# Kernel optimization log

Hardware: AMD Instinct MI355X
Metric: run time of the kernel (lower is better)

Reference implementation:

```python
import jax, jax.numpy as jnp
import numpy as np

N_NODES = 500_000
N_GRAPHS = 8192
HIDDEN = 256


def setup_inputs() -> dict:
    key = jax.random.key(0)
    k1, k2, k3, k4, k5, k6, k7 = jax.random.split(key, 7)
    h = jax.random.normal(k1, (N_NODES, HIDDEN), dtype=jnp.float32)
    node_mult = jax.random.uniform(k2, (N_NODES,), dtype=jnp.float32) * 3.0 + 0.5
    pressure = jax.random.uniform(k3, (N_GRAPHS,), dtype=jnp.float32) * 300.0
    attn_weight = jax.random.normal(k4, (HIDDEN,), dtype=jnp.float32) * (1.0 / np.sqrt(HIDDEN))
    attn_bias = jax.random.normal(k5, (1,), dtype=jnp.float32) * 0.01
    W_pressure = jax.random.normal(k6, (HIDDEN,), dtype=jnp.float32) * 0.02
    batch = jnp.sort(jax.random.randint(k7, (N_NODES,), 0, N_GRAPHS, dtype=jnp.int32))
    return {
        "h": h,
        "node_mult": node_mult,
        "pressure": pressure,
        "attn_weight": attn_weight,
        "attn_bias": attn_bias,
        "W_pressure": W_pressure,
        "batch": batch,
        "n_graphs": N_GRAPHS,
    }


def reference(h, node_mult, pressure, attn_weight, attn_bias, W_pressure, batch, n_graphs):
    # h: [N, H], node_mult: [N], batch: [N] int segment ids, pressure: [G]
    # Multiplicity-weighted mean pool
    total_mult = jax.ops.segment_sum(node_mult, batch, num_segments=n_graphs)  # [G]
    total_mult = jnp.maximum(total_mult, 1e-8)
    w_mean = node_mult / total_mult[batch]  # [N]
    mean_pool = jax.ops.segment_sum(h * w_mean[:, None], batch, num_segments=n_graphs)  # [G, H]

    # Segment max pool (empty segments -> -inf, matching torch full(-inf) init)
    max_pool = jax.ops.segment_max(h, batch, num_segments=n_graphs)  # [G, H]

    # Attention scores with log-multiplicity bias, then segment softmax
    raw_scores = h @ attn_weight + attn_bias[0] + jnp.log(jnp.maximum(node_mult, 1.0))  # [N]
    seg_max = jax.ops.segment_max(raw_scores, batch, num_segments=n_graphs)  # [G]
    exp_s = jnp.exp(raw_scores - seg_max[batch])  # [N]
    denom = jax.ops.segment_sum(exp_s, batch, num_segments=n_graphs)  # [G]
    attn_w = exp_s / denom[batch]  # [N]
    attn_pool = jax.ops.segment_sum(h * attn_w[:, None], batch, num_segments=n_graphs)  # [G, H]

    combined_mean = 0.5 * (mean_pool + attn_pool)  # [G, H]
    p_norm = (pressure / 300.0)[:, None]  # [G, 1]
    combined_mean = combined_mean + p_norm * W_pressure[None, :]
    return jnp.concatenate([combined_mean, max_pool], axis=-1)  # [G, 2H]
```

## Files before the change

### kernel.cpp

```cpp
#include <hip/hip_runtime.h>
#include <math.h>

#define HIDDEN 256
#define CHUNK 8

typedef float fx4 __attribute__((ext_vector_type(4)));

__global__ __launch_bounds__(256) void seg_starts_kernel(
    const int* __restrict__ batch, int* __restrict__ starts, int N, int G) {
  int i = blockIdx.x * blockDim.x + threadIdx.x;
  if (i >= N) return;
  int b = batch[i];
  int prev = (i == 0) ? -1 : batch[i - 1];
  for (int g = prev + 1; g <= b; ++g) starts[g] = i;
  if (i == N - 1) {
    for (int g = b + 1; g <= G; ++g) starts[g] = N;
  }
}

__global__ __launch_bounds__(256) void pool_kernel(
    const float* __restrict__ h, const float* __restrict__ node_mult,
    const float* __restrict__ pressure, const float* __restrict__ attn_weight,
    const float* __restrict__ attn_bias, const float* __restrict__ W_pressure,
    const int* __restrict__ starts, float* __restrict__ out, int G) {
  const int wave = threadIdx.x >> 6;
  const int lane = threadIdx.x & 63;
  const int g = blockIdx.x * 4 + wave;
  if (g >= G) return;

  const int start = starts[g];
  const int end = starts[g + 1];

  const fx4 w4 = *reinterpret_cast<const fx4*>(attn_weight + 4 * lane);
  const float bias = attn_bias[0];

  fx4 attn  = (fx4)(0.f);
  fx4 meanv = (fx4)(0.f);
  fx4 maxv  = (fx4)(-INFINITY);
  float m = -INFINITY;
  float denom = 0.f;
  float tmult = 0.f;

  int i = start;
  for (; i + CHUNK <= end; i += CHUNK) {
    fx4 hv[CHUNK];
    float mult[CHUNK];
#pragma unroll
    for (int j = 0; j < CHUNK; ++j) {
      hv[j] = __builtin_nontemporal_load(
          reinterpret_cast<const fx4*>(h + (size_t)(i + j) * HIDDEN + 4 * lane));
      mult[j] = node_mult[i + j];
    }

    float p[CHUNK];
#pragma unroll
    for (int j = 0; j < CHUNK; ++j)
      p[j] = hv[j].x * w4.x + hv[j].y * w4.y + hv[j].z * w4.z + hv[j].w * w4.w;

#pragma unroll
    for (int off = 32; off >= 1; off >>= 1) {
#pragma unroll
      for (int j = 0; j < CHUNK; ++j) p[j] += __shfl_xor(p[j], off, 64);
    }

    float s[CHUNK];
#pragma unroll
    for (int j = 0; j < CHUNK; ++j)
      s[j] = p[j] + bias + __logf(fmaxf(mult[j], 1.f));

    float cmax = s[0];
#pragma unroll
    for (int j = 1; j < CHUNK; ++j) cmax = fmaxf(cmax, s[j]);

    if (cmax > m) {
      const float scale = __expf(m - cmax);
      denom *= scale;
      attn *= scale;
      m = cmax;
    }

#pragma unroll
    for (int j = 0; j < CHUNK; ++j) {
      const float e = __expf(s[j] - m);
      denom += e;
      attn += hv[j] * e;
      meanv += hv[j] * mult[j];
      maxv.x = fmaxf(maxv.x, hv[j].x);  maxv.y = fmaxf(maxv.y, hv[j].y);
      maxv.z = fmaxf(maxv.z, hv[j].z);  maxv.w = fmaxf(maxv.w, hv[j].w);
      tmult += mult[j];
    }
  }

  for (; i < end; ++i) {
    const fx4 hv = __builtin_nontemporal_load(
        reinterpret_cast<const fx4*>(h + (size_t)i * HIDDEN + 4 * lane));
    const float mult = node_mult[i];

    float p = hv.x * w4.x + hv.y * w4.y + hv.z * w4.z + hv.w * w4.w;
#pragma unroll
    for (int off = 32; off >= 1; off >>= 1) p += __shfl_xor(p, off, 64);

    const float score = p + bias + __logf(fmaxf(mult, 1.f));

    if (score > m) {
      const float scale = __expf(m - score);
      denom *= scale;
      attn *= scale;
      m = score;
    }
    const float e = __expf(score - m);
    denom += e;
    attn += hv * e;
    meanv += hv * mult;
    maxv.x = fmaxf(maxv.x, hv.x);  maxv.y = fmaxf(maxv.y, hv.y);
    maxv.z = fmaxf(maxv.z, hv.z);  maxv.w = fmaxf(maxv.w, hv.w);
    tmult += mult;
  }

  const float inv_tm  = 1.f / fmaxf(tmult, 1e-8f);
  const float inv_den = (denom > 0.f) ? 1.f / denom : 0.f;
  const float p_norm  = pressure[g] * (1.f / 300.f);
  const fx4 wp4 = *reinterpret_cast<const fx4*>(W_pressure + 4 * lane);

  fx4 res = 0.5f * (meanv * inv_tm + attn * inv_den) + p_norm * wp4;

  float* outg = out + (size_t)g * (2 * HIDDEN);
  *reinterpret_cast<fx4*>(outg + 4 * lane) = res;
  *reinterpret_cast<fx4*>(outg + HIDDEN + 4 * lane) = maxv;
}

extern "C" void kernel_launch(void* const* d_in, const int* in_sizes, int n_in,
                              void* d_out, int out_size, void* d_ws, size_t ws_size,
                              hipStream_t stream) {
  const float* h           = (const float*)d_in[0];
  const float* node_mult   = (const float*)d_in[1];
  const float* pressure    = (const float*)d_in[2];
  const float* attn_weight = (const float*)d_in[3];
  const float* attn_bias   = (const float*)d_in[4];
  const float* W_pressure  = (const float*)d_in[5];
  const int*   batch       = (const int*)d_in[6];

  const int N = in_sizes[1];
  const int G = in_sizes[2];

  int* starts = (int*)d_ws;
  float* out = (float*)d_out;

  seg_starts_kernel<<<(N + 255) / 256, 256, 0, stream>>>(batch, starts, N, G);
  pool_kernel<<<(G + 3) / 4, 256, 0, stream>>>(h, node_mult, pressure,
                                               attn_weight, attn_bias,
                                               W_pressure, starts, out, G);
}
```

Before: 103.7 us.

## Split each segment across two waves and merge partial softmax states in LDS

Each graph segment is now handled by two waves, each covering half of the full 8-node chunks. The partial online-softmax, mean, max and multiplicity state is merged through shared memory after a block barrier. The scalar tail loop is replaced by one padded, masked chunk processed by the first wave. This doubles the waves in flight to hide memory latency on an HBM-bound reduction, at the cost of a barrier, LDS traffic and uneven work between the two halves.

Result: faster. 100.4 us (-3.2%).

```diff
diff --git a/kernel.cpp b/kernel.cpp
--- a/kernel.cpp
+++ b/kernel.cpp
@@ -23,13 +23,21 @@
     const float* __restrict__ pressure, const float* __restrict__ attn_weight,
     const float* __restrict__ attn_bias, const float* __restrict__ W_pressure,
     const int* __restrict__ starts, float* __restrict__ out, int G) {
-  const int wave = threadIdx.x >> 6;
-  const int lane = threadIdx.x & 63;
-  const int g = blockIdx.x * 4 + wave;
-  if (g >= G) return;
-
-  const int start = starts[g];
-  const int end = starts[g + 1];
+  const int wave  = threadIdx.x >> 6;
+  const int lane  = threadIdx.x & 63;
+  const int gslot = wave >> 1;
+  const int sub   = wave & 1;
+  const int g = blockIdx.x * 2 + gslot;
+  const bool active = (g < G);
+
+  __shared__ float s_m[2], s_d[2], s_t[2];
+  __shared__ fx4 s_attn[2][64], s_mean[2][64], s_max[2][64];
+
+  int start = 0, end = 0;
+  if (active) { start = starts[g]; end = starts[g + 1]; }
+  const int total = end - start;
+  const int nfull = total / CHUNK;
+  const int rem   = total - nfull * CHUNK;
 
   const fx4 w4 = *reinterpret_cast<const fx4*>(attn_weight + 4 * lane);
   const float bias = attn_bias[0];
@@ -41,8 +49,11 @@
   float denom = 0.f;
   float tmult = 0.f;
 
-  int i = start;
-  for (; i + CHUNK <= end; i += CHUNK) {
+  const int c_lo = (sub == 0) ? 0 : nfull / 2;
+  const int c_hi = (sub == 0) ? nfull / 2 : nfull;
+
+  for (int c = c_lo; c < c_hi; ++c) {
+    const int i = start + c * CHUNK;
     fx4 hv[CHUNK];
     float mult[CHUNK];
 #pragma unroll
@@ -91,42 +102,96 @@
     }
   }
 
-  for (; i < end; ++i) {
-    const fx4 hv = __builtin_nontemporal_load(
-        reinterpret_cast<const fx4*>(h + (size_t)i * HIDDEN + 4 * lane));
-    const float mult = node_mult[i];
-
-    float p = hv.x * w4.x + hv.y * w4.y + hv.z * w4.z + hv.w * w4.w;
-#pragma unroll
-    for (int off = 32; off >= 1; off >>= 1) p += __shfl_xor(p, off, 64);
-
-    const float score = p + bias + __logf(fmaxf(mult, 1.f));
-
-    if (score > m) {
-      const float scale = __expf(m - score);
+  if (sub == 0 && rem > 0) {
+    const int base = start + nfull * CHUNK;
+    fx4 hv[CHUNK];
+    float mult[CHUNK];
+#pragma unroll
+    for (int j = 0; j < CHUNK; ++j) {
+      const int idx = base + ((j < rem) ? j : rem - 1);
+      hv[j] = __builtin_nontemporal_load(
+          reinterpret_cast<const fx4*>(h + (size_t)idx * HIDDEN + 4 * lane));
+      mult[j] = (j < rem) ? node_mult[base + j] : 0.f;
+    }
+
+    float p[CHUNK];
+#pragma unroll
+    for (int j = 0; j < CHUNK; ++j)
+      p[j] = hv[j].x * w4.x + hv[j].y * w4.y + hv[j].z * w4.z + hv[j].w * w4.w;
+
+#pragma unroll
+    for (int off = 32; off >= 1; off >>= 1) {
+#pragma unroll
+      for (int j = 0; j < CHUNK; ++j) p[j] += __shfl_xor(p[j], off, 64);
+    }
+
+    float s[CHUNK];
+#pragma unroll
+    for (int j = 0; j < CHUNK; ++j)
+      s[j] = (j < rem) ? (p[j] + bias + __logf(fmaxf(mult[j], 1.f))) : -INFINITY;
+
+    float cmax = s[0];
+#pragma unroll
+    for (int j = 1; j < CHUNK; ++j) cmax = fmaxf(cmax, s[j]);
+
+    if (cmax > m) {
+      const float scale = __expf(m - cmax);
       denom *= scale;
       attn *= scale;
-      m = score;
-    }
-    const float e = __expf(score - m);
-    denom += e;
-    attn += hv * e;
-    meanv += hv * mult;
-    maxv.x = fmaxf(maxv.x, hv.x);  maxv.y = fmaxf(maxv.y, hv.y);
-    maxv.z = fmaxf(maxv.z, hv.z);  maxv.w = fmaxf(maxv.w, hv.w);
-    tmult += mult;
-  }
-
-  const float inv_tm  = 1.f / fmaxf(tmult, 1e-8f);
-  const float inv_den = (denom > 0.f) ? 1.f / denom : 0.f;
-  const float p_norm  = pressure[g] * (1.f / 300.f);
-  const fx4 wp4 = *reinterpret_cast<const fx4*>(W_pressure + 4 * lane);
-
-  fx4 res = 0.5f * (meanv * inv_tm + attn * inv_den) + p_norm * wp4;
-
-  float* outg = out + (size_t)g * (2 * HIDDEN);
-  *reinterpret_cast<fx4*>(outg + 4 * lane) = res;
-  *reinterpret_cast<fx4*>(outg + HIDDEN + 4 * lane) = maxv;
+      m = cmax;
+    }
+
+#pragma unroll
+    for (int j = 0; j < CHUNK; ++j) {
+      const float e = __expf(s[j] - m);
+      denom += e;
+      attn += hv[j] * e;
+      meanv += hv[j] * mult[j];
+      const bool v = (j < rem);
+      maxv.x = fmaxf(maxv.x, v ? hv[j].x : -INFINITY);
+      maxv.y = fmaxf(maxv.y, v ? hv[j].y : -INFINITY);
+      maxv.z = fmaxf(maxv.z, v ? hv[j].z : -INFINITY);
+      maxv.w = fmaxf(maxv.w, v ? hv[j].w : -INFINITY);
+      tmult += mult[j];
+    }
+  }
+
+  if (sub == 1) {
+    if (lane == 0) { s_m[gslot] = m; s_d[gslot] = denom; s_t[gslot] = tmult; }
+    s_attn[gslot][lane] = attn;
+    s_mean[gslot][lane] = meanv;
+    s_max[gslot][lane]  = maxv;
+  }
+  __syncthreads();
+
+  if (active && sub == 0) {
+    const float m1 = s_m[gslot], d1 = s_d[gslot], t1 = s_t[gslot];
+    const fx4 attn1 = s_attn[gslot][lane];
+    const fx4 mean1 = s_mean[gslot][lane];
+    const fx4 max1  = s_max[gslot][lane];
+
+    const float M = fmaxf(m, m1);
+    const float sc0 = (m  == -INFINITY) ? 0.f : __expf(m  - M);
+    const float sc1 = (m1 == -INFINITY) ? 0.f : __expf(m1 - M);
+    const float D = denom * sc0 + d1 * sc1;
+    const fx4 A = attn * sc0 + attn1 * sc1;
+    const fx4 Me = meanv + mean1;
+    fx4 Mx;
+    Mx.x = fmaxf(maxv.x, max1.x);  Mx.y = fmaxf(maxv.y, max1.y);
+    Mx.z = fmaxf(maxv.z, max1.z);  Mx.w = fmaxf(maxv.w, max1.w);
+    const float T = tmult + t1;
+
+    const float inv_tm  = 1.f / fmaxf(T, 1e-8f);
+    const float inv_den = (D > 0.f) ? 1.f / D : 0.f;
+    const float p_norm  = pressure[g] * (1.f / 300.f);
+    const fx4 wp4 = *reinterpret_cast<const fx4*>(W_pressure + 4 * lane);
+
+    fx4 res = 0.5f * (Me * inv_tm + A * inv_den) + p_norm * wp4;
+
+    float* outg = out + (size_t)g * (2 * HIDDEN);
+    *reinterpret_cast<fx4*>(outg + 4 * lane) = res;
+    *reinterpret_cast<fx4*>(outg + HIDDEN + 4 * lane) = Mx;
+  }
 }
 
 extern "C" void kernel_launch(void* const* d_in, const int* in_sizes, int n_in,
@@ -147,7 +212,7 @@
   float* out = (float*)d_out;
 
   seg_starts_kernel<<<(N + 255) / 256, 256, 0, stream>>>(batch, starts, N, G);
-  pool_kernel<<<(G + 3) / 4, 256, 0, stream>>>(h, node_mult, pressure,
+  pool_kernel<<<(G + 1) / 2, 256, 0, stream>>>(h, node_mult, pressure,
                                                attn_weight, attn_bias,
                                                W_pressure, starts, out, G);
 }
```
